# Kernel optimization log

Hardware: AMD Instinct MI355X
Metric: run time of the kernel (lower is better)

## Reference

```python
import jax, jax.numpy as jnp
import numpy as np

N_NODES = 50000
N_EDGES = 800000
F_IN = 256
F_OUT = 256


def setup_inputs() -> dict:
    key = jax.random.key(0)
    k1, k2, k3, k4, k5 = jax.random.split(key, 5)
    x = jax.random.normal(k1, (N_NODES, F_IN), dtype=jnp.float32)
    edge_index = jax.random.randint(k2, (2, N_EDGES), 0, N_NODES, dtype=jnp.int64)
    C_values = jax.random.uniform(k3, (N_EDGES,), dtype=jnp.float32)
    # nn.Linear(input_dim, output_dim) parameters
    W = jax.random.normal(k4, (F_OUT, F_IN), dtype=jnp.float32) / np.sqrt(F_IN)
    b = jax.random.normal(k5, (F_OUT,), dtype=jnp.float32) * 0.01
    return {"x": x, "edge_index": edge_index, "C_values": C_values, "W": W, "b": b}


def reference(x, edge_index, C_values, W, b):
    # gcn_norm(add_self_loops=False): deg = row-sum of edge weights,
    # w_norm[e] = deg[row]^-1/2 * w[e] * deg[col]^-1/2
    row, col = edge_index[0], edge_index[1]
    n = x.shape[0]
    deg = jax.ops.segment_sum(C_values, row, num_segments=n)  # [N]
    deg_inv_sqrt = jnp.where(deg > 0, jax.lax.rsqrt(jnp.where(deg > 0, deg, 1.0)), 0.0)
    w_norm = deg_inv_sqrt[row] * C_values * deg_inv_sqrt[col]  # [E]
    # SpMM: prop_x[i] = sum_{e: row[e]=i} w_norm[e] * x[col[e]]
    prop_x = jax.ops.segment_sum(w_norm[:, None] * x[col], row, num_segments=n)  # [N, F_in]
    # dense linear transform
    return prop_x @ W.T + b  # [N, F_out]
```

## Files before the change

### kernel.cpp

```cpp
#include <hip/hip_runtime.h>
#include <hip/hip_bf16.h>

#define NN 50000
#define NE 800000
#define FD 256
#define NN_PAD 50048
#define SCAN_B 196

typedef __attribute__((ext_vector_type(8))) short bf16x8;
typedef __attribute__((ext_vector_type(16))) short short16;
typedef __attribute__((ext_vector_type(4))) float f32x4;
typedef unsigned long long ull;

__device__ __forceinline__ short f2bf(float f) {
    union { float f; unsigned u; } v; v.f = f;
    unsigned r = v.u + 0x7fffu + ((v.u >> 16) & 1u);
    return (short)(r >> 16);
}
__device__ __forceinline__ float bf2f(unsigned short u) {
    union { unsigned u; float f; } v; v.u = ((unsigned)u) << 16;
    return v.f;
}

__global__ void count_deg_kernel(const int* __restrict__ row, const float* __restrict__ cv,
                                 ull* __restrict__ dc) {
    int e = blockIdx.x * blockDim.x + threadIdx.x;
    if (e < NE) {
        int r = row[e];
        unsigned cf = (unsigned)(cv[e] * 16777216.0f + 0.5f);
        atomicAdd(&dc[r], (1ULL << 40) | (ull)cf);
    }
}

__device__ __forceinline__ int block_excl_scan256(int v, int tid) {
    __shared__ int ws[4];
    int lane = tid & 63, wv = tid >> 6;
    int incl = v;
#pragma unroll
    for (int off = 1; off < 64; off <<= 1) {
        int t = __shfl_up(incl, off);
        if (lane >= off) incl += t;
    }
    if (lane == 63) ws[wv] = incl;
    __syncthreads();
    int acc = 0;
#pragma unroll
    for (int k = 0; k < 4; ++k) if (k < wv) acc += ws[k];
    return acc + incl - v;
}

__global__ void sum_dinv_kernel(const ull* __restrict__ dc, float* __restrict__ dinv,
                                int* __restrict__ bsum) {
    int i = blockIdx.x * 256 + threadIdx.x;
    ull v = (i < NN) ? dc[i] : 0ULL;
    int cnt = (int)(v >> 40);
    ull df = v & ((1ULL << 40) - 1);
    int lane = threadIdx.x & 63, wv = threadIdx.x >> 6;
    int s = cnt;
#pragma unroll
    for (int off = 1; off < 64; off <<= 1) s += __shfl_xor(s, off);
    __shared__ int ws[4];
    if (lane == 0) ws[wv] = s;
    __syncthreads();
    if (threadIdx.x == 0) bsum[blockIdx.x] = ws[0] + ws[1] + ws[2] + ws[3];
    if (i < NN) {
        float d = (float)df * (1.0f / 16777216.0f);
        dinv[i] = (df > 0) ? rsqrtf(d) : 0.f;
    }
}

__global__ void scan_bsum_kernel(int* __restrict__ bsum) {
    int tid = threadIdx.x;
    int v = (tid < SCAN_B) ? bsum[tid] : 0;
    int excl = block_excl_scan256(v, tid);
    if (tid < SCAN_B) bsum[tid] = excl;
}

__global__ void write_rs_kernel(const ull* __restrict__ dc, const int* __restrict__ bsum,
                                int* __restrict__ rs, int* __restrict__ cursor) {
    int i = blockIdx.x * 256 + threadIdx.x;
    int v = (i < NN) ? (int)(dc[i] >> 40) : 0;
    int excl = block_excl_scan256(v, threadIdx.x) + bsum[blockIdx.x];
    if (i < NN) { rs[i] = excl; cursor[i] = excl; }
    if (i == NN - 1) rs[NN] = excl + v;
}

__global__ void convert_kernel(const float* __restrict__ x, const float* __restrict__ W,
                               const float* __restrict__ dinv,
                               short* __restrict__ xbs, short* __restrict__ Wb) {
    size_t i = ((size_t)blockIdx.x * blockDim.x + threadIdx.x) * 4;
    const size_t NX = (size_t)NN * FD;
    if (i < NX) {
        float dr = dinv[i >> 8];
        float4 v = *(const float4*)(x + i);
        short* d = xbs + i;
        d[0] = f2bf(v.x * dr); d[1] = f2bf(v.y * dr);
        d[2] = f2bf(v.z * dr); d[3] = f2bf(v.w * dr);
    } else {
        size_t j = i - NX;
        if (j < (size_t)FD * FD) {
            float4 v = *(const float4*)(W + j);
            short* d = Wb + j;
            d[0] = f2bf(v.x); d[1] = f2bf(v.y); d[2] = f2bf(v.z); d[3] = f2bf(v.w);
        }
    }
}

__global__ void bucket_kernel(const int* __restrict__ row, const int* __restrict__ col,
                              const float* __restrict__ cv,
                              int* __restrict__ cursor, ull* __restrict__ e_cw) {
    int e = blockIdx.x * blockDim.x + threadIdx.x;
    if (e >= NE) return;
    int r = row[e], c = col[e];
    int idx = atomicAdd(&cursor[r], 1);
    union { float f; unsigned u; } wu; wu.f = cv[e];
    e_cw[idx] = ((ull)wu.u << 32) | (unsigned)c;
}

__global__ __launch_bounds__(256) void fused_kernel(
        const short* __restrict__ xbs, const ull* __restrict__ e_cw,
        const int* __restrict__ rs, const float* __restrict__ dinv,
        const short* __restrict__ Wb, const float* __restrict__ bias,
        float* __restrict__ out) {
    __shared__ short A[16][264];
    int tid = threadIdx.x, lane = tid & 63, wv = tid >> 6;
    int q = lane >> 4, i = lane & 15;
    int nbase = blockIdx.x * 16;
    int n = nbase + wv * 4 + q;

    int s = rs[n], en = rs[n + 1];
    float dr = dinv[n];
    float acc[16];
#pragma unroll
    for (int k = 0; k < 16; ++k) acc[k] = 0.f;

    const short* xb_i = xbs + i * 16;
    int e = s;
    for (; e + 2 <= en; e += 2) {
        ull cw0 = e_cw[e], cw1 = e_cw[e + 1];
        int c0 = (int)(unsigned)cw0, c1 = (int)(unsigned)cw1;
        union { unsigned u; float f; } u0, u1;
        u0.u = (unsigned)(cw0 >> 32); u1.u = (unsigned)(cw1 >> 32);
        short16 v0 = *(const short16*)(xb_i + (size_t)c0 * FD);
        short16 v1 = *(const short16*)(xb_i + (size_t)c1 * FD);
#pragma unroll
        for (int k = 0; k < 16; ++k) acc[k] += u0.f * bf2f((unsigned short)v0[k]);
#pragma unroll
        for (int k = 0; k < 16; ++k) acc[k] += u1.f * bf2f((unsigned short)v1[k]);
    }
    if (e < en) {
        ull cw0 = e_cw[e];
        int c0 = (int)(unsigned)cw0;
        union { unsigned u; float f; } u0; u0.u = (unsigned)(cw0 >> 32);
        short16 v0 = *(const short16*)(xb_i + (size_t)c0 * FD);
#pragma unroll
        for (int k = 0; k < 16; ++k) acc[k] += u0.f * bf2f((unsigned short)v0[k]);
    }

    bf16x8 lo, hi;
#pragma unroll
    for (int k = 0; k < 8; ++k) {
        lo[k] = f2bf(acc[k] * dr);
        hi[k] = f2bf(acc[k + 8] * dr);
    }
    *(bf16x8*)&A[wv * 4 + q][i * 16] = lo;
    *(bf16x8*)&A[wv * 4 + q][i * 16 + 8] = hi;
    __syncthreads();

    int m = lane & 15, g = lane >> 4;
    f32x4 acc0 = {0,0,0,0}, acc1 = {0,0,0,0}, acc2 = {0,0,0,0}, acc3 = {0,0,0,0};
    const short* w0 = Wb + (size_t)(wv * 64 + 0  + m) * FD;
    const short* w1 = Wb + (size_t)(wv * 64 + 16 + m) * FD;
    const short* w2 = Wb + (size_t)(wv * 64 + 32 + m) * FD;
    const short* w3 = Wb + (size_t)(wv * 64 + 48 + m) * FD;
#pragma unroll
    for (int ks = 0; ks < 8; ++ks) {
        int ko = ks * 32 + g * 8;
        bf16x8 af = *(const bf16x8*)&A[m][ko];
        bf16x8 b0 = *(const bf16x8*)(w0 + ko);
        bf16x8 b1 = *(const bf16x8*)(w1 + ko);
        bf16x8 b2 = *(const bf16x8*)(w2 + ko);
        bf16x8 b3 = *(const bf16x8*)(w3 + ko);
        acc0 = __builtin_amdgcn_mfma_f32_16x16x32_bf16(af, b0, acc0, 0, 0, 0);
        acc1 = __builtin_amdgcn_mfma_f32_16x16x32_bf16(af, b1, acc1, 0, 0, 0);
        acc2 = __builtin_amdgcn_mfma_f32_16x16x32_bf16(af, b2, acc2, 0, 0, 0);
        acc3 = __builtin_amdgcn_mfma_f32_16x16x32_bf16(af, b3, acc3, 0, 0, 0);
    }
#pragma unroll
    for (int nt = 0; nt < 4; ++nt) {
        f32x4 a = nt == 0 ? acc0 : nt == 1 ? acc1 : nt == 2 ? acc2 : acc3;
        int c = wv * 64 + nt * 16 + m;
        float bv = bias[c];
#pragma unroll
        for (int r = 0; r < 4; ++r) {
            out[(size_t)(nbase + g * 4 + r) * FD + c] = a[r] + bv;
        }
    }
}

extern "C" void kernel_launch(void* const* d_in, const int* in_sizes, int n_in,
                              void* d_out, int out_size, void* d_ws, size_t ws_size,
                              hipStream_t stream) {
    const float* x  = (const float*)d_in[0];
    const int*   ei = (const int*)d_in[1];
    const float* cv = (const float*)d_in[2];
    const float* W  = (const float*)d_in[3];
    const float* b  = (const float*)d_in[4];
    float* out = (float*)d_out;

    const int* row = ei;
    const int* col = ei + NE;

    ull*   dc     = (ull*)d_ws;
    ull*   e_cw   = dc + NN_PAD;
    short* xbs    = (short*)(e_cw + NE);
    short* Wb     = xbs + (size_t)NN * FD;
    float* dinv   = (float*)(Wb + (size_t)FD * FD);
    int*   rs     = (int*)(dinv + NN_PAD);
    int*   cursor = rs + NN_PAD;
    int*   bsum   = cursor + NN_PAD;

    hipMemsetAsync(dc, 0, NN_PAD * sizeof(ull), stream);

    count_deg_kernel<<<(NE + 255) / 256, 256, 0, stream>>>(row, cv, dc);
    sum_dinv_kernel<<<SCAN_B, 256, 0, stream>>>(dc, dinv, bsum);
    scan_bsum_kernel<<<1, 256, 0, stream>>>(bsum);
    write_rs_kernel<<<SCAN_B, 256, 0, stream>>>(dc, bsum, rs, cursor);
    const size_t NCONV = ((size_t)NN * FD + (size_t)FD * FD) / 4;
    convert_kernel<<<(NCONV + 255) / 256, 256, 0, stream>>>(x, W, dinv, xbs, Wb);
    bucket_kernel<<<(NE + 255) / 256, 256, 0, stream>>>(row, col, cv, cursor, e_cw);

    fused_kernel<<<NN / 16, 256, 0, stream>>>(xbs, e_cw, rs, dinv, Wb, b, out);
}
```

Before: 220.4 us.

## Balance edges across thread groups and pack edge index with quantized weight

The fused SpMM kernel now gives each 16-thread group an equal contiguous chunk of the block's edges instead of one node each, and flushes partial sums into a shared fp32 tile with LDS atomics at node boundaries. This is meant to remove load imbalance from varying node degrees. Edge records shrink from 64-bit (fp32 weight plus column) to 32-bit, with the weight quantized to 16 bits and the column in 16 bits, which halves edge-list traffic and allows 4-wide edge loads. The 16-bit column field cannot hold indices at or above 65536, which is fine for the 50000-node graph. Risks are reduced weight precision, extra LDS atomic traffic, and the zero-init and extra syncs.

```diff
diff --git a/kernel.cpp b/kernel.cpp
--- a/kernel.cpp
+++ b/kernel.cpp
@@ -6,6 +6,7 @@
 #define FD 256
 #define NN_PAD 50048
 #define SCAN_B 196
+#define NPB 16
 
 typedef __attribute__((ext_vector_type(8))) short bf16x8;
 typedef __attribute__((ext_vector_type(16))) short short16;
@@ -108,63 +109,106 @@
 
 __global__ void bucket_kernel(const int* __restrict__ row, const int* __restrict__ col,
                               const float* __restrict__ cv,
-                              int* __restrict__ cursor, ull* __restrict__ e_cw) {
+                              int* __restrict__ cursor, unsigned* __restrict__ e_cw) {
     int e = blockIdx.x * blockDim.x + threadIdx.x;
     if (e >= NE) return;
     int r = row[e], c = col[e];
     int idx = atomicAdd(&cursor[r], 1);
-    union { float f; unsigned u; } wu; wu.f = cv[e];
-    e_cw[idx] = ((ull)wu.u << 32) | (unsigned)c;
+    unsigned cf = (unsigned)fminf(cv[e] * 65536.0f + 0.5f, 65535.0f);
+    e_cw[idx] = (cf << 16) | (unsigned)c;
 }
 
 __global__ __launch_bounds__(256) void fused_kernel(
-        const short* __restrict__ xbs, const ull* __restrict__ e_cw,
+        const short* __restrict__ xbs, const unsigned* __restrict__ e_cw,
         const int* __restrict__ rs, const float* __restrict__ dinv,
         const short* __restrict__ Wb, const float* __restrict__ bias,
         float* __restrict__ out) {
-    __shared__ short A[16][264];
+    __shared__ float Af[NPB][264];
+    __shared__ short Ab[NPB][264];
+    __shared__ int rsl[NPB + 1];
     int tid = threadIdx.x, lane = tid & 63, wv = tid >> 6;
-    int q = lane >> 4, i = lane & 15;
-    int nbase = blockIdx.x * 16;
-    int n = nbase + wv * 4 + q;
-
-    int s = rs[n], en = rs[n + 1];
-    float dr = dinv[n];
-    float acc[16];
-#pragma unroll
-    for (int k = 0; k < 16; ++k) acc[k] = 0.f;
-
-    const short* xb_i = xbs + i * 16;
-    int e = s;
-    for (; e + 2 <= en; e += 2) {
-        ull cw0 = e_cw[e], cw1 = e_cw[e + 1];
-        int c0 = (int)(unsigned)cw0, c1 = (int)(unsigned)cw1;
-        union { unsigned u; float f; } u0, u1;
-        u0.u = (unsigned)(cw0 >> 32); u1.u = (unsigned)(cw1 >> 32);
-        short16 v0 = *(const short16*)(xb_i + (size_t)c0 * FD);
-        short16 v1 = *(const short16*)(xb_i + (size_t)c1 * FD);
-#pragma unroll
-        for (int k = 0; k < 16; ++k) acc[k] += u0.f * bf2f((unsigned short)v0[k]);
-#pragma unroll
-        for (int k = 0; k < 16; ++k) acc[k] += u1.f * bf2f((unsigned short)v1[k]);
-    }
-    if (e < en) {
-        ull cw0 = e_cw[e];
-        int c0 = (int)(unsigned)cw0;
-        union { unsigned u; float f; } u0; u0.u = (unsigned)(cw0 >> 32);
-        short16 v0 = *(const short16*)(xb_i + (size_t)c0 * FD);
-#pragma unroll
-        for (int k = 0; k < 16; ++k) acc[k] += u0.f * bf2f((unsigned short)v0[k]);
-    }
-
-    bf16x8 lo, hi;
-#pragma unroll
-    for (int k = 0; k < 8; ++k) {
-        lo[k] = f2bf(acc[k] * dr);
-        hi[k] = f2bf(acc[k + 8] * dr);
-    }
-    *(bf16x8*)&A[wv * 4 + q][i * 16] = lo;
-    *(bf16x8*)&A[wv * 4 + q][i * 16 + 8] = hi;
+    int nbase = blockIdx.x * NPB;
+    int qg = tid >> 4;
+    int i  = tid & 15;
+
+    for (int t = tid; t < NPB * 264; t += 256) ((float*)Af)[t] = 0.f;
+    if (tid <= NPB) rsl[tid] = rs[nbase + tid];
+    __syncthreads();
+
+    int eb = rsl[0], ee = rsl[NPB];
+    int ne = ee - eb;
+    int C  = (ne + NPB - 1) >> 4;
+    int e    = eb + qg * C;
+    int eend = min(e + C, ee);
+
+    if (e < eend) {
+        int nidx = 0;
+        while (rsl[nidx + 1] <= e) ++nidx;
+        int nb = rsl[nidx + 1];
+        const short* xq = xbs + i * 16;
+
+        float acc[16];
+#pragma unroll
+        for (int k = 0; k < 16; ++k) acc[k] = 0.f;
+
+        auto flush_adv = [&]() {
+#pragma unroll
+            for (int k = 0; k < 16; ++k) {
+                atomicAdd(&Af[nidx][i * 16 + k], acc[k]);
+                acc[k] = 0.f;
+            }
+            ++nidx; nb = rsl[nidx + 1];
+        };
+        auto accum = [&](short16 v, float cvf) {
+#pragma unroll
+            for (int k = 0; k < 16; ++k)
+                acc[k] = fmaf(cvf, bf2f((unsigned short)v[k]), acc[k]);
+        };
+
+        while (e < eend && (e & 3)) {
+            unsigned cw = e_cw[e];
+            short16 v = *(const short16*)(xq + (size_t)(cw & 0xFFFFu) * FD);
+            while (e >= nb) flush_adv();
+            accum(v, (float)(cw >> 16));
+            ++e;
+        }
+        for (; e + 4 <= eend; e += 4) {
+            uint4 cw4 = *(const uint4*)(e_cw + e);
+            short16 v0 = *(const short16*)(xq + (size_t)(cw4.x & 0xFFFFu) * FD);
+            short16 v1 = *(const short16*)(xq + (size_t)(cw4.y & 0xFFFFu) * FD);
+            short16 v2 = *(const short16*)(xq + (size_t)(cw4.z & 0xFFFFu) * FD);
+            short16 v3 = *(const short16*)(xq + (size_t)(cw4.w & 0xFFFFu) * FD);
+            while (e     >= nb) flush_adv();
+            accum(v0, (float)(cw4.x >> 16));
+            while (e + 1 >= nb) flush_adv();
+            accum(v1, (float)(cw4.y >> 16));
+            while (e + 2 >= nb) flush_adv();
+            accum(v2, (float)(cw4.z >> 16));
+            while (e + 3 >= nb) flush_adv();
+            accum(v3, (float)(cw4.w >> 16));
+        }
+        for (; e < eend; ++e) {
+            unsigned cw = e_cw[e];
+            short16 v = *(const short16*)(xq + (size_t)(cw & 0xFFFFu) * FD);
+            while (e >= nb) flush_adv();
+            accum(v, (float)(cw >> 16));
+        }
+#pragma unroll
+        for (int k = 0; k < 16; ++k) atomicAdd(&Af[nidx][i * 16 + k], acc[k]);
+    }
+    __syncthreads();
+
+    {
+        float s = dinv[nbase + qg] * (1.0f / 65536.0f);
+        bf16x8 lo, hi;
+#pragma unroll
+        for (int k = 0; k < 8; ++k) {
+            lo[k] = f2bf(Af[qg][i * 16 + k] * s);
+            hi[k] = f2bf(Af[qg][i * 16 + 8 + k] * s);
+        }
+        *(bf16x8*)&Ab[qg][i * 16] = lo;
+        *(bf16x8*)&Ab[qg][i * 16 + 8] = hi;
+    }
     __syncthreads();
 
     int m = lane & 15, g = lane >> 4;
@@ -176,7 +220,7 @@
 #pragma unroll
     for (int ks = 0; ks < 8; ++ks) {
         int ko = ks * 32 + g * 8;
-        bf16x8 af = *(const bf16x8*)&A[m][ko];
+        bf16x8 af = *(const bf16x8*)&Ab[m][ko];
         bf16x8 b0 = *(const bf16x8*)(w0 + ko);
         bf16x8 b1 = *(const bf16x8*)(w1 + ko);
         bf16x8 b2 = *(const bf16x8*)(w2 + ko);
@@ -211,14 +255,14 @@
     const int* row = ei;
     const int* col = ei + NE;
 
-    ull*   dc     = (ull*)d_ws;
-    ull*   e_cw   = dc + NN_PAD;
-    short* xbs    = (short*)(e_cw + NE);
-    short* Wb     = xbs + (size_t)NN * FD;
-    float* dinv   = (float*)(Wb + (size_t)FD * FD);
-    int*   rs     = (int*)(dinv + NN_PAD);
-    int*   cursor = rs + NN_PAD;
-    int*   bsum   = cursor + NN_PAD;
+    ull*      dc     = (ull*)d_ws;
+    unsigned* e_cw   = (unsigned*)(dc + NN_PAD);
+    short*    xbs    = (short*)(e_cw + NE);
+    short*    Wb     = xbs + (size_t)NN * FD;
+    float*    dinv   = (float*)(Wb + (size_t)FD * FD);
+    int*      rs     = (int*)(dinv + NN_PAD);
+    int*      cursor = rs + NN_PAD;
+    int*      bsum   = cursor + NN_PAD;
 
     hipMemsetAsync(dc, 0, NN_PAD * sizeof(ull), stream);
 
@@ -230,5 +274,5 @@
     convert_kernel<<<(NCONV + 255) / 256, 256, 0, stream>>>(x, W, dinv, xbs, Wb);
     bucket_kernel<<<(NE + 255) / 256, 256, 0, stream>>>(row, col, cv, cursor, e_cw);
 
-    fused_kernel<<<NN / 16, 256, 0, stream>>>(xbs, e_cw, rs, dinv, Wb, b, out);
-}
+    fused_kernel<<<NN / NPB, 256, 0, stream>>>(xbs, e_cw, rs, dinv, Wb, b, out);
+}
```

Result: slower. 268.1 us (+21.6%).
